# Kernel optimization log

Measured on AMD Instinct MI355X. Metric: run time of the kernel, lower is better.

The kernel has to match this reference:

```python
import jax, jax.numpy as jnp
import numpy as np

N = 50000
E = 400000
F_IN = 5
H = 8
C1, C2, C3 = 64, 32, 16
NEG_SLOPE = 0.2


def setup_inputs() -> dict:
    key = jax.random.key(0)
    ks = jax.random.split(key, 16)
    s = 0.1  # small init scale
    return {
        "x": jax.random.normal(ks[0], (N, F_IN), jnp.float32),
        "edge_index": jax.random.randint(ks[1], (2, E), 0, N, jnp.int64),
        "edge_weight": jax.random.uniform(ks[2], (E,), jnp.float32),
        "W1": jax.random.normal(ks[3], (F_IN, H * C1), jnp.float32) * s,
        "a_src1": jax.random.normal(ks[4], (H, C1), jnp.float32) * s,
        "a_dst1": jax.random.normal(ks[5], (H, C1), jnp.float32) * s,
        "b1": jnp.zeros((H * C1,), jnp.float32),
        "W2": jax.random.normal(ks[6], (H * C1, H * C2), jnp.float32) * s,
        "a_src2": jax.random.normal(ks[7], (H, C2), jnp.float32) * s,
        "a_dst2": jax.random.normal(ks[8], (H, C2), jnp.float32) * s,
        "b2": jnp.zeros((H * C2,), jnp.float32),
        "Wg": jax.random.normal(ks[9], (H * C2, C3), jnp.float32) * s,
        "bg": jnp.zeros((C3,), jnp.float32),
        "Wfc": jax.random.normal(ks[10], (C3, 1), jnp.float32) * s,
        "bfc": jnp.zeros((1,), jnp.float32),
    }


def _gat_layer(x, W, a_src, a_dst, b, src, dst, n, heads, ch):
    # PyG GATConv (concat=True), eval mode (dropout off), self-loops already in src/dst.
    h = (x @ W).reshape(n, heads, ch)                      # (N, H, C)
    e_s = jnp.sum(h * a_src, axis=-1)                      # (N, H)
    e_d = jnp.sum(h * a_dst, axis=-1)                      # (N, H)
    e = jax.nn.leaky_relu(e_s[src] + e_d[dst], NEG_SLOPE)  # (Etot, H)
    m = jax.ops.segment_max(e, dst, num_segments=n)
    m = jnp.where(jnp.isfinite(m), m, 0.0)                 # guard empty segments
    ex = jnp.exp(e - m[dst])
    den = jax.ops.segment_sum(ex, dst, num_segments=n)
    alpha = ex / (den[dst] + 1e-16)                        # softmax over in-edges
    out = jax.ops.segment_sum(h[src] * alpha[..., None], dst, num_segments=n)
    return out.reshape(n, heads * ch) + b


def _gcn_layer(x, W, b, src, dst, w_full, n):
    # PyG GCNConv with gcn_norm: D^{-1/2} A_hat D^{-1/2}, self-loop weight 1.
    deg = jax.ops.segment_sum(w_full, dst, num_segments=n)
    dinv = jnp.where(deg > 0, jax.lax.rsqrt(deg), 0.0)
    norm = dinv[src] * w_full * dinv[dst]                  # (Etot,)
    h = x @ W                                              # (N, C3)
    out = jax.ops.segment_sum(h[src] * norm[:, None], dst, num_segments=n)
    return out + b


def reference(x, edge_index, edge_weight, W1, a_src1, a_dst1, b1,
              W2, a_src2, a_dst2, b2, Wg, bg, Wfc, bfc):
    n = x.shape[0]
    loops = jnp.arange(n, dtype=edge_index.dtype)
    src = jnp.concatenate([edge_index[0], loops])
    dst = jnp.concatenate([edge_index[1], loops])
    w_full = jnp.concatenate([edge_weight, jnp.ones((n,), edge_weight.dtype)])

    h = _gat_layer(x, W1, a_src1, a_dst1, b1, src, dst, n, H, C1)
    h = jax.nn.elu(h)
    h = _gat_layer(h, W2, a_src2, a_dst2, b2, src, dst, n, H, C2)
    h = jax.nn.elu(h)
    h = _gcn_layer(h, Wg, bg, src, dst, w_full, n)
    h = jax.nn.elu(h)
    out = jax.nn.sigmoid(h @ Wfc + bfc)                    # (N, 1)
    return out
```

## Files before the change

### kernel.cpp

```cpp
#include <hip/hip_runtime.h>
#include <hip/hip_bf16.h>
#include <float.h>
#include <math.h>

#define N_NODES 50000
#define N_EDGES 400000
#define ETOT    (N_EDGES + N_NODES)
#define F_IN    5
#define HEADS   8
#define C1      64
#define C2      32
#define C3      16
#define HC1     (HEADS * C1)
#define HC2     (HEADS * C2)
#define NEG_SLOPE 0.2f
#define NCHUNK  ((N_NODES + 255) / 256)
#define NH8     (N_NODES * HEADS)
#define MPAD    (((N_NODES + 63) / 64) * 64)
#define GCOLS   (HC2 + 16)
#define PACKBLK ((GCOLS * HC1) / 256)
#define SCATBLK ((ETOT + 255) / 256)
#define ES1BLK  ((NH8 + 255) / 256)
#define DEGBLK  SCATBLK
#define XPBLK   ((N_NODES * 8 + 255) / 256)

typedef short bf16x8 __attribute__((ext_vector_type(8)));
typedef float f32x4  __attribute__((ext_vector_type(4)));
typedef unsigned short ushort_t;
typedef unsigned short ushort8_t __attribute__((ext_vector_type(8)));

__device__ __forceinline__ float eluf(float x) {
    return x > 0.f ? x : (expf(x) - 1.f);
}
__device__ __forceinline__ float bf2f(unsigned short u) {
    union { unsigned int i; float f; } v; v.i = ((unsigned int)u) << 16; return v.f;
}
__device__ __forceinline__ unsigned short f2bf(float f) {
    __hip_bfloat16 b = __float2bfloat16(f);
    return *(unsigned short*)&b;
}
__device__ __forceinline__ float softnum(float es, float ed) {
    float v = es + ed;
    v = v > 0.f ? v : NEG_SLOPE * v;
    return expf(v);
}

__global__ void k_deg(const int* __restrict__ ei, const float* __restrict__ ew,
                      int* degi, float* degf,
                      const float* __restrict__ x, float* __restrict__ xp8) {
    if (blockIdx.x < DEGBLK) {
        int i = blockIdx.x * blockDim.x + threadIdx.x;
        if (i >= ETOT) return;
        int d   = (i < N_EDGES) ? ei[N_EDGES + i] : (i - N_EDGES);
        float w = (i < N_EDGES) ? ew[i] : 1.f;
        atomicAdd(&degi[d], 1);
        atomicAdd(&degf[d], w);
    } else {
        int g = (blockIdx.x - DEGBLK) * 256 + threadIdx.x;
        if (g >= N_NODES * 8) return;
        int n = g >> 3, f = g & 7;
        xp8[g] = (f < F_IN) ? x[n * F_IN + f] : 0.f;
    }
}

__global__ void k_scan_a(const int* __restrict__ deg, int* __restrict__ part) {
    __shared__ int lds[256];
    int t = threadIdx.x;
    int i = blockIdx.x * 256 + t;
    lds[t] = (i < N_NODES) ? deg[i] : 0;
    __syncthreads();
    for (int off = 128; off >= 1; off >>= 1) {
        if (t < off) lds[t] += lds[t + off];
        __syncthreads();
    }
    if (t == 0) part[blockIdx.x] = lds[0];
}

__global__ void k_scan_b(int* part) {
    __shared__ int lds[256];
    int t = threadIdx.x;
    int v = (t < NCHUNK) ? part[t] : 0;
    lds[t] = v;
    __syncthreads();
    for (int off = 1; off < 256; off <<= 1) {
        int x = (t >= off) ? lds[t - off] : 0;
        __syncthreads();
        lds[t] += x;
        __syncthreads();
    }
    if (t < NCHUNK) part[t] = lds[t] - v;
}

__global__ void k_scan_c(const int* __restrict__ deg, const int* __restrict__ part,
                         int* __restrict__ offs,
                         const float* __restrict__ degf, float* __restrict__ dinv) {
    __shared__ int lds[256];
    int t = threadIdx.x;
    int i = blockIdx.x * 256 + t;
    int v = (i < N_NODES) ? deg[i] : 0;
    lds[t] = v;
    __syncthreads();
    for (int off = 1; off < 256; off <<= 1) {
        int x = (t >= off) ? lds[t - off] : 0;
        __syncthreads();
        lds[t] += x;
        __syncthreads();
    }
    int excl = part[blockIdx.x] + lds[t] - v;
    if (i < N_NODES) {
        offs[i] = excl;
        float dd = degf[i];
        dinv[i] = dd > 0.f ? rsqrtf(dd) : 0.f;
    }
    if (i == N_NODES - 1) offs[N_NODES] = excl + v;
}

__global__ void k_prep(const float* __restrict__ W2,
                       const float* __restrict__ a_src2, const float* __restrict__ a_dst2,
                       ushort_t* __restrict__ W2X,
                       const float* __restrict__ W1,
                       const float* __restrict__ a_src1, const float* __restrict__ a_dst1,
                       float* __restrict__ as1f, float* __restrict__ ad1f) {
    if (blockIdx.x < PACKBLK) {
        int idx = blockIdx.x * 256 + threadIdx.x;
        int c = idx >> 9;
        int k = idx & 511;
        float v;
        if (c < HC2) {
            v = W2[(size_t)k * HC2 + c];
        } else {
            int h = (c - HC2) & 7;
            const float* av = (c < HC2 + 8) ? a_src2 : a_dst2;
            v = 0.f;
#pragma unroll 8
            for (int j = 0; j < C2; j++)
                v += W2[(size_t)k * HC2 + h * C2 + j] * av[h * C2 + j];
        }
        W2X[idx] = f2bf(v);
    } else {
        int idx = threadIdx.x;
        if (idx >= HEADS * F_IN) return;
        int h = idx / F_IN, f = idx % F_IN;
        float s = 0.f, d = 0.f;
        for (int c = 0; c < C1; c++) {
            float w = W1[f * HC1 + h * C1 + c];
            s += w * a_src1[h * C1 + c];
            d += w * a_dst1[h * C1 + c];
        }
        as1f[idx] = s;
        ad1f[idx] = d;
    }
}

__global__ void k_scatter_es1(const int* __restrict__ ei, const int* __restrict__ offs,
                              int* cursor, int2* __restrict__ csr,
                              const float* __restrict__ ew, const float* __restrict__ dinv,
                              const float* __restrict__ x,
                              const float* __restrict__ as1f, const float* __restrict__ ad1f,
                              float* __restrict__ es, float* __restrict__ ed) {
    if (blockIdx.x < SCATBLK) {
        int i = blockIdx.x * 256 + threadIdx.x;
        if (i >= ETOT) return;
        int s, d;
        float w;
        if (i < N_EDGES) { s = ei[i]; d = ei[N_EDGES + i]; w = ew[i]; }
        else             { s = d = i - N_EDGES; w = 1.f; }
        float nrm = dinv[s] * w * dinv[d];
        int pos = offs[d] + atomicAdd(&cursor[d], 1);
        csr[pos] = make_int2(s, __float_as_int(nrm));
    } else {
        int g = (blockIdx.x - SCATBLK) * 256 + threadIdx.x;
        if (g >= NH8) return;
        int n = g >> 3, h = g & 7;
        float vs = 0.f, vd = 0.f;
#pragma unroll
        for (int f = 0; f < F_IN; f++) {
            float xv = x[n * F_IN + f];
            vs += xv * as1f[h * F_IN + f];
            vd += xv * ad1f[h * F_IN + f];
        }
        es[g] = vs;
        ed[g] = vd;
    }
}

__global__ void k_agg_x(const float* __restrict__ xp8,
                        const float* __restrict__ es1, const float* __restrict__ ed1,
                        const int* __restrict__ offs, const int2* __restrict__ csr,
                        float* __restrict__ aggx) {
    int g = blockIdx.x * blockDim.x + threadIdx.x;
    if (g >= NH8) return;
    int d = g >> 3, h = g & 7;
    float edv = ed1[g];
    int k0 = offs[d], k1 = offs[d + 1];
    float a0 = 0.f, a1 = 0.f, a2 = 0.f, a3 = 0.f, a4 = 0.f, exsum = 0.f;
    int k = k0;
    if (k + 1 < k1) {
        int2 c0 = csr[k], c1 = csr[k + 1];
        for (; k + 3 < k1; k += 2) {
            int2 n0 = csr[k + 2], n1 = csr[k + 3];
            float x0 = softnum(es1[c0.x * HEADS + h], edv);
            float x1 = softnum(es1[c1.x * HEADS + h], edv);
            float4 A0 = *(const float4*)(xp8 + (size_t)c0.x * 8);
            float  B0 = xp8[(size_t)c0.x * 8 + 4];
            float4 A1 = *(const float4*)(xp8 + (size_t)c1.x * 8);
            float  B1 = xp8[(size_t)c1.x * 8 + 4];
            a0 += x0 * A0.x + x1 * A1.x;
            a1 += x0 * A0.y + x1 * A1.y;
            a2 += x0 * A0.z + x1 * A1.z;
            a3 += x0 * A0.w + x1 * A1.w;
            a4 += x0 * B0   + x1 * B1;
            exsum += x0 + x1;
            c0 = n0; c1 = n1;
        }
        {
            float x0 = softnum(es1[c0.x * HEADS + h], edv);
            float x1 = softnum(es1[c1.x * HEADS + h], edv);
            float4 A0 = *(const float4*)(xp8 + (size_t)c0.x * 8);
            float  B0 = xp8[(size_t)c0.x * 8 + 4];
            float4 A1 = *(const float4*)(xp8 + (size_t)c1.x * 8);
            float  B1 = xp8[(size_t)c1.x * 8 + 4];
            a0 += x0 * A0.x + x1 * A1.x;
            a1 += x0 * A0.y + x1 * A1.y;
            a2 += x0 * A0.z + x1 * A1.z;
            a3 += x0 * A0.w + x1 * A1.w;
            a4 += x0 * B0   + x1 * B1;
            exsum += x0 + x1;
            k += 2;
        }
    }
    if (k < k1) {
        int2 c0 = csr[k];
        float x0 = softnum(es1[c0.x * HEADS + h], edv);
        float4 A0 = *(const float4*)(xp8 + (size_t)c0.x * 8);
        float  B0 = xp8[(size_t)c0.x * 8 + 4];
        a0 += x0 * A0.x;
        a1 += x0 * A0.y;
        a2 += x0 * A0.z;
        a3 += x0 * A0.w;
        a4 += x0 * B0;
        exsum += x0;
    }
    float inv = 1.f / (exsum + 1e-16f);
    aggx[0 * NH8 + g] = a0 * inv;
    aggx[1 * NH8 + g] = a1 * inv;
    aggx[2 * NH8 + g] = a2 * inv;
    aggx[3 * NH8 + g] = a3 * inv;
    aggx[4 * NH8 + g] = a4 * inv;
}

__global__ __launch_bounds__(256) void k_expand(const float* __restrict__ aggx,
                                                const float* __restrict__ W1,
                                                const float* __restrict__ b1,
                                                ushort_t* __restrict__ x2bf) {
    int wave = threadIdx.x >> 6;
    int j    = threadIdx.x & 63;
    int n    = blockIdx.x * 4 + wave;
    if (n >= N_NODES) return;
    int h = j >> 3;
    int g = n * HEADS + h;
    float av[F_IN];
#pragma unroll
    for (int f = 0; f < F_IN; f++) av[f] = aggx[f * NH8 + g];

    const float* w1p = W1 + j * 8;
    float4 s0 = *(const float4*)(b1 + j * 8);
    float4 s1 = *(const float4*)(b1 + j * 8 + 4);
#pragma unroll
    for (int f = 0; f < F_IN; f++) {
        float4 w0  = *(const float4*)(w1p + f * HC1);
        float4 w1v = *(const float4*)(w1p + f * HC1 + 4);
        s0.x += av[f] * w0.x;  s0.y += av[f] * w0.y;
        s0.z += av[f] * w0.z;  s0.w += av[f] * w0.w;
        s1.x += av[f] * w1v.x; s1.y += av[f] * w1v.y;
        s1.z += av[f] * w1v.z; s1.w += av[f] * w1v.w;
    }
    ushort8_t o;
    o[0] = f2bf(eluf(s0.x)); o[1] = f2bf(eluf(s0.y));
    o[2] = f2bf(eluf(s0.z)); o[3] = f2bf(eluf(s0.w));
    o[4] = f2bf(eluf(s1.x)); o[5] = f2bf(eluf(s1.y));
    o[6] = f2bf(eluf(s1.z)); o[7] = f2bf(eluf(s1.w));
    *(ushort8_t*)(x2bf + (size_t)n * HC1 + j * 8) = o;
}

__global__ __launch_bounds__(256, 3) void k_gemm_mfma(const short* __restrict__ A,
                                                      const short* __restrict__ W2X,
                                                      ushort_t* __restrict__ h2bf,
                                                      float* __restrict__ es2,
                                                      float* __restrict__ ed2) {
    __shared__ short Bs[GCOLS * 32];
    int t    = threadIdx.x;
    int wave = t >> 6;
    int lane = t & 63;
    int lo   = lane & 15;
    int quad = lane >> 4;
    int m0   = blockIdx.x * 64 + wave * 16;
    const short* ap = A + (size_t)(m0 + lo) * HC1 + quad * 8;

    f32x4 acc[17];
#pragma unroll
    for (int f = 0; f < 17; f++) acc[f] = (f32x4){0.f, 0.f, 0.f, 0.f};

    for (int idx = t; idx < GCOLS * 4; idx += 256) {
        int c = idx >> 2, q = idx & 3;
        int s = (q + c + (c >> 2)) & 3;
        *(bf16x8*)(Bs + c * 32 + s * 8) = *(const bf16x8*)(W2X + (size_t)c * HC1 + q * 8);
    }
    __syncthreads();

#pragma unroll 1
    for (int k0 = 0; k0 < HC1; k0 += 32) {
        int nk = k0 + 32;
        bf16x8 pre[5];
        if (nk < HC1) {
#pragma unroll
            for (int j = 0; j < 5; j++) {
                int idx = t + j * 256;
                if (idx < GCOLS * 4) {
                    int c = idx >> 2, q = idx & 3;
                    pre[j] = *(const bf16x8*)(W2X + (size_t)c * HC1 + nk + q * 8);
                }
            }
        }
        bf16x8 aF = *(const bf16x8*)(ap + k0);
#pragma unroll
        for (int f = 0; f < 17; f++) {
            int c = f * 16 + lo;
            int s = (quad + c + (c >> 2)) & 3;
            bf16x8 bF = *(const bf16x8*)(Bs + c * 32 + s * 8);
            acc[f] = __builtin_amdgcn_mfma_f32_16x16x32_bf16(aF, bF, acc[f], 0, 0, 0);
        }
        __syncthreads();
        if (nk < HC1) {
#pragma unroll
            for (int j = 0; j < 5; j++) {
                int idx = t + j * 256;
                if (idx < GCOLS * 4) {
                    int c = idx >> 2, q = idx & 3;
                    int s = (q + c + (c >> 2)) & 3;
                    *(bf16x8*)(Bs + c * 32 + s * 8) = pre[j];
                }
            }
            __syncthreads();
        }
    }

    int rowb = m0 + quad * 4;
#pragma unroll
    for (int f = 0; f < 16; f++) {
#pragma unroll
        for (int r = 0; r < 4; r++) {
            int row = rowb + r;
            if (row < N_NODES)
                h2bf[(size_t)row * HC2 + f * 16 + lo] = f2bf(acc[f][r]);
        }
    }
#pragma unroll
    for (int r = 0; r < 4; r++) {
        int row = rowb + r;
        if (row < N_NODES) {
            if (lo < 8) es2[row * HEADS + lo]       = acc[16][r];
            else        ed2[row * HEADS + (lo - 8)] = acc[16][r];
        }
    }
}

__global__ __launch_bounds__(256) void k_gat_agg2(const ushort_t* __restrict__ h2bf,
                                                  const float* __restrict__ es2,
                                                  const float* __restrict__ ed2,
                                                  const int* __restrict__ offs,
                                                  const int2* __restrict__ csr,
                                                  const float* __restrict__ b2,
                                                  ushort_t* __restrict__ x3bf) {
    int wave = threadIdx.x >> 6;
    int lane = threadIdx.x & 63;
    int d = blockIdx.x * 4 + wave;
    if (d >= N_NODES) return;
    int c4 = lane * 4;
    int h  = lane >> 3;
    float edv = ed2[d * HEADS + h];
    int k0 = offs[d], k1 = offs[d + 1];
    float acc0 = 0.f, acc1 = 0.f, acc2 = 0.f, acc3 = 0.f, exsum = 0.f;
    int k = k0;
    for (; k + 3 < k1; k += 4) {
        int2 e0 = csr[k], e1 = csr[k + 1], e2 = csr[k + 2], e3 = csr[k + 3];
        float r0 = es2[e0.x * HEADS + h];
        float r1 = es2[e1.x * HEADS + h];
        float r2 = es2[e2.x * HEADS + h];
        float r3 = es2[e3.x * HEADS + h];
        ushort4 v0 = *(const ushort4*)(h2bf + (size_t)e0.x * HC2 + c4);
        ushort4 v1 = *(const ushort4*)(h2bf + (size_t)e1.x * HC2 + c4);
        ushort4 v2 = *(const ushort4*)(h2bf + (size_t)e2.x * HC2 + c4);
        ushort4 v3 = *(const ushort4*)(h2bf + (size_t)e3.x * HC2 + c4);
        float x0 = softnum(r0, edv);
        float x1 = softnum(r1, edv);
        float x2 = softnum(r2, edv);
        float x3 = softnum(r3, edv);
        acc0 += x0 * bf2f(v0.x) + x1 * bf2f(v1.x) + x2 * bf2f(v2.x) + x3 * bf2f(v3.x);
        acc1 += x0 * bf2f(v0.y) + x1 * bf2f(v1.y) + x2 * bf2f(v2.y) + x3 * bf2f(v3.y);
        acc2 += x0 * bf2f(v0.z) + x1 * bf2f(v1.z) + x2 * bf2f(v2.z) + x3 * bf2f(v3.z);
        acc3 += x0 * bf2f(v0.w) + x1 * bf2f(v1.w) + x2 * bf2f(v2.w) + x3 * bf2f(v3.w);
        exsum += (x0 + x1) + (x2 + x3);
    }
    for (; k < k1; k++) {
        int2 e0 = csr[k];
        float x0 = softnum(es2[e0.x * HEADS + h], edv);
        ushort4 v0 = *(const ushort4*)(h2bf + (size_t)e0.x * HC2 + c4);
        acc0 += x0 * bf2f(v0.x);
        acc1 += x0 * bf2f(v0.y);
        acc2 += x0 * bf2f(v0.z);
        acc3 += x0 * bf2f(v0.w);
        exsum += x0;
    }
    float inv = 1.f / (exsum + 1e-16f);
    float4 bias = *(const float4*)(b2 + c4);
    ushort4 o;
    o.x = f2bf(eluf(acc0 * inv + bias.x));
    o.y = f2bf(eluf(acc1 * inv + bias.y));
    o.z = f2bf(eluf(acc2 * inv + bias.z));
    o.w = f2bf(eluf(acc3 * inv + bias.w));
    *(ushort4*)(x3bf + (size_t)d * HC2 + c4) = o;
}

__global__ __launch_bounds__(256) void k_hg(const ushort_t* __restrict__ x3bf,
                                            const float* __restrict__ Wg,
                                            float* __restrict__ hg) {
    __shared__ float xs[16 * 260];
    int n0 = blockIdx.x * 16;
    int t  = threadIdx.x;
    for (int q = t; q < 16 * HC2 / 4; q += 256) {
        int r  = q >> 6;
        int cc = (q & 63) * 4;
        int n  = n0 + r;
        ushort4 v = make_ushort4(0, 0, 0, 0);
        if (n < N_NODES) v = *(const ushort4*)(x3bf + (size_t)n * HC2 + cc);
        xs[r * 260 + cc + 0] = bf2f(v.x);
        xs[r * 260 + cc + 1] = bf2f(v.y);
        xs[r * 260 + cc + 2] = bf2f(v.z);
        xs[r * 260 + cc + 3] = bf2f(v.w);
    }
    __syncthreads();
    int r = t >> 4, c = t & 15;
    const float* xr = xs + r * 260;
    float acc = 0.f;
#pragma unroll 8
    for (int k = 0; k < HC2; k += 4) {
        float4 v = *(const float4*)(xr + k);
        acc += v.x * Wg[(k + 0) * C3 + c];
        acc += v.y * Wg[(k + 1) * C3 + c];
        acc += v.z * Wg[(k + 2) * C3 + c];
        acc += v.w * Wg[(k + 3) * C3 + c];
    }
    int n = n0 + r;
    if (n < N_NODES) hg[(size_t)n * C3 + c] = acc;
}

__global__ __launch_bounds__(256) void k_gcn_out(const float* __restrict__ hg,
                                                 const int* __restrict__ offs,
                                                 const int2* __restrict__ csr,
                                                 const float* __restrict__ bg,
                                                 const float* __restrict__ Wfc,
                                                 const float* __restrict__ bfc,
                                                 float* __restrict__ out) {
    int t = threadIdx.x;
    int r = t >> 4, c = t & 15;
    int d = blockIdx.x * 16 + r;
    float val = 0.f;
    if (d < N_NODES) {
        int k0 = offs[d], k1 = offs[d + 1];
        float acc = 0.f;
        int k = k0;
        if (k + 1 < k1) {
            int2 e0 = csr[k], e1 = csr[k + 1];
            for (; k + 3 < k1; k += 2) {
                int2 n0 = csr[k + 2], n1 = csr[k + 3];
                acc += hg[(size_t)e0.x * C3 + c] * __int_as_float(e0.y);
                acc += hg[(size_t)e1.x * C3 + c] * __int_as_float(e1.y);
                e0 = n0; e1 = n1;
            }
            acc += hg[(size_t)e0.x * C3 + c] * __int_as_float(e0.y);
            acc += hg[(size_t)e1.x * C3 + c] * __int_as_float(e1.y);
            k += 2;
        }
        if (k < k1) {
            int2 e0 = csr[k];
            acc += hg[(size_t)e0.x * C3 + c] * __int_as_float(e0.y);
        }
        val = eluf(acc + bg[c]);
    }
    float z = val * Wfc[c];
#pragma unroll
    for (int off = 8; off >= 1; off >>= 1) z += __shfl_xor(z, off, 16);
    if (c == 0 && d < N_NODES) out[d] = 1.f / (1.f + expf(-(z + bfc[0])));
}

extern "C" void kernel_launch(void* const* d_in, const int* in_sizes, int n_in,
                              void* d_out, int out_size, void* d_ws, size_t ws_size,
                              hipStream_t stream) {
    const float* x       = (const float*)d_in[0];
    const int*   ei      = (const int*)  d_in[1];
    const float* ew      = (const float*)d_in[2];
    const float* W1      = (const float*)d_in[3];
    const float* a_src1  = (const float*)d_in[4];
    const float* a_dst1  = (const float*)d_in[5];
    const float* b1      = (const float*)d_in[6];
    const float* W2      = (const float*)d_in[7];
    const float* a_src2  = (const float*)d_in[8];
    const float* a_dst2  = (const float*)d_in[9];
    const float* b2      = (const float*)d_in[10];
    const float* Wg      = (const float*)d_in[11];
    const float* bg      = (const float*)d_in[12];
    const float* Wfc     = (const float*)d_in[13];
    const float* bfc     = (const float*)d_in[14];
    float* out = (float*)d_out;

    char* w = (char*)d_ws;
    size_t off = 0;
    auto alloc = [&](size_t bytes) -> void* {
        void* p = w + off;
        off = (off + bytes + 255) & ~(size_t)255;
        return p;
    };
    ushort_t* x2bf = (ushort_t*)alloc((size_t)MPAD * HC1 * 2);
    ushort_t* W2X  = (ushort_t*)alloc((size_t)GCOLS * HC1 * 2);
    ushort_t* h2bf = (ushort_t*)alloc((size_t)N_NODES * HC2 * 2);
    ushort_t* x3bf = (ushort_t*)alloc((size_t)N_NODES * HC2 * 2);
    float* hg     = (float*)alloc((size_t)N_NODES * C3 * 4);
    float* aggx   = (float*)alloc((size_t)F_IN * NH8 * 4);
    float* es1    = (float*)alloc((size_t)NH8 * 4);
    float* ed1    = (float*)alloc((size_t)NH8 * 4);
    float* es2    = (float*)alloc((size_t)NH8 * 4);
    float* ed2    = (float*)alloc((size_t)NH8 * 4);
    float* as1f   = (float*)alloc((size_t)HEADS * F_IN * 4);
    float* ad1f   = (float*)alloc((size_t)HEADS * F_IN * 4);
    float* degf   = (float*)alloc((size_t)N_NODES * 4);
    int*   degi   = (int*)  alloc((size_t)N_NODES * 4);
    int*   cursor = (int*)  alloc((size_t)N_NODES * 4);
    char*  zero_end = w + off;
    int*   offs   = (int*)  alloc((size_t)(N_NODES + 1) * 4);
    int*   part   = (int*)  alloc(256 * 4);
    int2*  csr    = (int2*) alloc((size_t)ETOT * 8);
    float* dinv   = (float*)alloc((size_t)N_NODES * 4);
    float* xp8    = (float*)alloc((size_t)N_NODES * 8 * 4);

    const int T = 256;
    hipMemsetAsync(degf, 0, (size_t)(zero_end - (char*)degf), stream);
    k_deg<<<dim3(DEGBLK + XPBLK), dim3(T), 0, stream>>>(ei, ew, degi, degf, x, xp8);
    k_scan_a<<<dim3(NCHUNK), dim3(256), 0, stream>>>(degi, part);
    k_scan_b<<<dim3(1), dim3(256), 0, stream>>>(part);
    k_scan_c<<<dim3(NCHUNK), dim3(256), 0, stream>>>(degi, part, offs, degf, dinv);
    k_prep<<<dim3(PACKBLK + 1), dim3(256), 0, stream>>>(
        W2, a_src2, a_dst2, W2X, W1, a_src1, a_dst1, as1f, ad1f);
    k_scatter_es1<<<dim3(SCATBLK + ES1BLK), dim3(256), 0, stream>>>(
        ei, offs, cursor, csr, ew, dinv, x, as1f, ad1f, es1, ed1);

    k_agg_x<<<dim3((NH8 + T - 1) / T), dim3(T), 0, stream>>>(xp8, es1, ed1, offs, csr, aggx);
    k_expand<<<dim3((N_NODES + 3) / 4), dim3(256), 0, stream>>>(aggx, W1, b1, x2bf);

    k_gemm_mfma<<<dim3(MPAD / 64), dim3(256), 0, stream>>>(
        (const short*)x2bf, (const short*)W2X, h2bf, es2, ed2);
    k_gat_agg2<<<dim3((N_NODES + 3) / 4), dim3(256), 0, stream>>>(
        h2bf, es2, ed2, offs, csr, b2, x3bf);

    k_hg<<<dim3((N_NODES + 15) / 16), dim3(256), 0, stream>>>(x3bf, Wg, hg);
    k_gcn_out<<<dim3((N_NODES + 15) / 16), dim3(256), 0, stream>>>(
        hg, offs, csr, bg, Wfc, bfc, out);
}
```

Baseline: 310.1 us.

## Fuse setup kernels, merge layer-1 aggregation with expansion, shrink agg2 blocks

Merges the degree count, x padding, W2X packing and es1/ed1 projection into one init kernel, with the per-head attention vectors computed in shared memory per block. The layer-1 softmax aggregation and the expansion through W1 become one kernel, so the aggregated features pass through LDS instead of a global aggx buffer. This cuts two launches and a global round trip. The layer-2 aggregation kernel now runs 128-thread blocks of two nodes each, which may change occupancy and tail behaviour. Each es block recomputes the small attention projections, a small amount of redundant work.

```diff
diff --git a/kernel.cpp b/kernel.cpp
--- a/kernel.cpp
+++ b/kernel.cpp
@@ -21,8 +21,11 @@
 #define PACKBLK ((GCOLS * HC1) / 256)
 #define SCATBLK ((ETOT + 255) / 256)
 #define ES1BLK  ((NH8 + 255) / 256)
-#define DEGBLK  SCATBLK
 #define XPBLK   ((N_NODES * 8 + 255) / 256)
+#define INIT_DEG  SCATBLK
+#define INIT_XP   (INIT_DEG + XPBLK)
+#define INIT_W2X  (INIT_XP + PACKBLK)
+#define INIT_TOT  (INIT_W2X + ES1BLK)
 
 typedef short bf16x8 __attribute__((ext_vector_type(8)));
 typedef float f32x4  __attribute__((ext_vector_type(4)));
@@ -45,84 +48,32 @@
     return expf(v);
 }
 
-__global__ void k_deg(const int* __restrict__ ei, const float* __restrict__ ew,
-                      int* degi, float* degf,
-                      const float* __restrict__ x, float* __restrict__ xp8) {
-    if (blockIdx.x < DEGBLK) {
-        int i = blockIdx.x * blockDim.x + threadIdx.x;
+__global__ void k_init(const int* __restrict__ ei, const float* __restrict__ ew,
+                       int* degi, float* degf,
+                       const float* __restrict__ x, float* __restrict__ xp8,
+                       const float* __restrict__ W2,
+                       const float* __restrict__ a_src2, const float* __restrict__ a_dst2,
+                       ushort_t* __restrict__ W2X,
+                       const float* __restrict__ W1,
+                       const float* __restrict__ a_src1, const float* __restrict__ a_dst1,
+                       float* __restrict__ es, float* __restrict__ ed) {
+    __shared__ float asl[HEADS * F_IN], adl[HEADS * F_IN];
+    int b = blockIdx.x;
+    int t = threadIdx.x;
+    if (b < INIT_DEG) {
+        int i = b * 256 + t;
         if (i >= ETOT) return;
         int d   = (i < N_EDGES) ? ei[N_EDGES + i] : (i - N_EDGES);
         float w = (i < N_EDGES) ? ew[i] : 1.f;
         atomicAdd(&degi[d], 1);
         atomicAdd(&degf[d], w);
-    } else {
-        int g = (blockIdx.x - DEGBLK) * 256 + threadIdx.x;
+    } else if (b < INIT_XP) {
+        int g = (b - INIT_DEG) * 256 + t;
         if (g >= N_NODES * 8) return;
         int n = g >> 3, f = g & 7;
         xp8[g] = (f < F_IN) ? x[n * F_IN + f] : 0.f;
-    }
-}
-
-__global__ void k_scan_a(const int* __restrict__ deg, int* __restrict__ part) {
-    __shared__ int lds[256];
-    int t = threadIdx.x;
-    int i = blockIdx.x * 256 + t;
-    lds[t] = (i < N_NODES) ? deg[i] : 0;
-    __syncthreads();
-    for (int off = 128; off >= 1; off >>= 1) {
-        if (t < off) lds[t] += lds[t + off];
-        __syncthreads();
-    }
-    if (t == 0) part[blockIdx.x] = lds[0];
-}
-
-__global__ void k_scan_b(int* part) {
-    __shared__ int lds[256];
-    int t = threadIdx.x;
-    int v = (t < NCHUNK) ? part[t] : 0;
-    lds[t] = v;
-    __syncthreads();
-    for (int off = 1; off < 256; off <<= 1) {
-        int x = (t >= off) ? lds[t - off] : 0;
-        __syncthreads();
-        lds[t] += x;
-        __syncthreads();
-    }
-    if (t < NCHUNK) part[t] = lds[t] - v;
-}
-
-__global__ void k_scan_c(const int* __restrict__ deg, const int* __restrict__ part,
-                         int* __restrict__ offs,
-                         const float* __restrict__ degf, float* __restrict__ dinv) {
-    __shared__ int lds[256];
-    int t = threadIdx.x;
-    int i = blockIdx.x * 256 + t;
-    int v = (i < N_NODES) ? deg[i] : 0;
-    lds[t] = v;
-    __syncthreads();
-    for (int off = 1; off < 256; off <<= 1) {
-        int x = (t >= off) ? lds[t - off] : 0;
-        __syncthreads();
-        lds[t] += x;
-        __syncthreads();
-    }
-    int excl = part[blockIdx.x] + lds[t] - v;
-    if (i < N_NODES) {
-        offs[i] = excl;
-        float dd = degf[i];
-        dinv[i] = dd > 0.f ? rsqrtf(dd) : 0.f;
-    }
-    if (i == N_NODES - 1) offs[N_NODES] = excl + v;
-}
-
-__global__ void k_prep(const float* __restrict__ W2,
-                       const float* __restrict__ a_src2, const float* __restrict__ a_dst2,
-                       ushort_t* __restrict__ W2X,
-                       const float* __restrict__ W1,
-                       const float* __restrict__ a_src1, const float* __restrict__ a_dst1,
-                       float* __restrict__ as1f, float* __restrict__ ad1f) {
-    if (blockIdx.x < PACKBLK) {
-        int idx = blockIdx.x * 256 + threadIdx.x;
+    } else if (b < INIT_W2X) {
+        int idx = (b - INIT_XP) * 256 + t;
         int c = idx >> 9;
         int k = idx & 511;
         float v;
@@ -138,149 +89,203 @@
         }
         W2X[idx] = f2bf(v);
     } else {
-        int idx = threadIdx.x;
-        if (idx >= HEADS * F_IN) return;
-        int h = idx / F_IN, f = idx % F_IN;
-        float s = 0.f, d = 0.f;
-        for (int c = 0; c < C1; c++) {
-            float w = W1[f * HC1 + h * C1 + c];
-            s += w * a_src1[h * C1 + c];
-            d += w * a_dst1[h * C1 + c];
-        }
-        as1f[idx] = s;
-        ad1f[idx] = d;
-    }
-}
-
-__global__ void k_scatter_es1(const int* __restrict__ ei, const int* __restrict__ offs,
-                              int* cursor, int2* __restrict__ csr,
-                              const float* __restrict__ ew, const float* __restrict__ dinv,
-                              const float* __restrict__ x,
-                              const float* __restrict__ as1f, const float* __restrict__ ad1f,
-                              float* __restrict__ es, float* __restrict__ ed) {
-    if (blockIdx.x < SCATBLK) {
-        int i = blockIdx.x * 256 + threadIdx.x;
-        if (i >= ETOT) return;
-        int s, d;
-        float w;
-        if (i < N_EDGES) { s = ei[i]; d = ei[N_EDGES + i]; w = ew[i]; }
-        else             { s = d = i - N_EDGES; w = 1.f; }
-        float nrm = dinv[s] * w * dinv[d];
-        int pos = offs[d] + atomicAdd(&cursor[d], 1);
-        csr[pos] = make_int2(s, __float_as_int(nrm));
-    } else {
-        int g = (blockIdx.x - SCATBLK) * 256 + threadIdx.x;
-        if (g >= NH8) return;
-        int n = g >> 3, h = g & 7;
-        float vs = 0.f, vd = 0.f;
-#pragma unroll
-        for (int f = 0; f < F_IN; f++) {
-            float xv = x[n * F_IN + f];
-            vs += xv * as1f[h * F_IN + f];
-            vd += xv * ad1f[h * F_IN + f];
-        }
-        es[g] = vs;
-        ed[g] = vd;
-    }
-}
-
-__global__ void k_agg_x(const float* __restrict__ xp8,
-                        const float* __restrict__ es1, const float* __restrict__ ed1,
-                        const int* __restrict__ offs, const int2* __restrict__ csr,
-                        float* __restrict__ aggx) {
-    int g = blockIdx.x * blockDim.x + threadIdx.x;
-    if (g >= NH8) return;
-    int d = g >> 3, h = g & 7;
-    float edv = ed1[g];
-    int k0 = offs[d], k1 = offs[d + 1];
-    float a0 = 0.f, a1 = 0.f, a2 = 0.f, a3 = 0.f, a4 = 0.f, exsum = 0.f;
-    int k = k0;
-    if (k + 1 < k1) {
-        int2 c0 = csr[k], c1 = csr[k + 1];
-        for (; k + 3 < k1; k += 2) {
-            int2 n0 = csr[k + 2], n1 = csr[k + 3];
-            float x0 = softnum(es1[c0.x * HEADS + h], edv);
-            float x1 = softnum(es1[c1.x * HEADS + h], edv);
-            float4 A0 = *(const float4*)(xp8 + (size_t)c0.x * 8);
-            float  B0 = xp8[(size_t)c0.x * 8 + 4];
-            float4 A1 = *(const float4*)(xp8 + (size_t)c1.x * 8);
-            float  B1 = xp8[(size_t)c1.x * 8 + 4];
-            a0 += x0 * A0.x + x1 * A1.x;
-            a1 += x0 * A0.y + x1 * A1.y;
-            a2 += x0 * A0.z + x1 * A1.z;
-            a3 += x0 * A0.w + x1 * A1.w;
-            a4 += x0 * B0   + x1 * B1;
-            exsum += x0 + x1;
-            c0 = n0; c1 = n1;
-        }
-        {
-            float x0 = softnum(es1[c0.x * HEADS + h], edv);
-            float x1 = softnum(es1[c1.x * HEADS + h], edv);
-            float4 A0 = *(const float4*)(xp8 + (size_t)c0.x * 8);
-            float  B0 = xp8[(size_t)c0.x * 8 + 4];
-            float4 A1 = *(const float4*)(xp8 + (size_t)c1.x * 8);
-            float  B1 = xp8[(size_t)c1.x * 8 + 4];
-            a0 += x0 * A0.x + x1 * A1.x;
-            a1 += x0 * A0.y + x1 * A1.y;
-            a2 += x0 * A0.z + x1 * A1.z;
-            a3 += x0 * A0.w + x1 * A1.w;
-            a4 += x0 * B0   + x1 * B1;
-            exsum += x0 + x1;
-            k += 2;
-        }
-    }
-    if (k < k1) {
-        int2 c0 = csr[k];
-        float x0 = softnum(es1[c0.x * HEADS + h], edv);
-        float4 A0 = *(const float4*)(xp8 + (size_t)c0.x * 8);
-        float  B0 = xp8[(size_t)c0.x * 8 + 4];
-        a0 += x0 * A0.x;
-        a1 += x0 * A0.y;
-        a2 += x0 * A0.z;
-        a3 += x0 * A0.w;
-        a4 += x0 * B0;
-        exsum += x0;
-    }
-    float inv = 1.f / (exsum + 1e-16f);
-    aggx[0 * NH8 + g] = a0 * inv;
-    aggx[1 * NH8 + g] = a1 * inv;
-    aggx[2 * NH8 + g] = a2 * inv;
-    aggx[3 * NH8 + g] = a3 * inv;
-    aggx[4 * NH8 + g] = a4 * inv;
-}
-
-__global__ __launch_bounds__(256) void k_expand(const float* __restrict__ aggx,
+        if (t < HEADS * F_IN) {
+            int h = t / F_IN, f = t % F_IN;
+            float s = 0.f, dv = 0.f;
+            for (int c = 0; c < C1; c++) {
+                float wv = W1[f * HC1 + h * C1 + c];
+                s  += wv * a_src1[h * C1 + c];
+                dv += wv * a_dst1[h * C1 + c];
+            }
+            asl[t] = s;
+            adl[t] = dv;
+        }
+        __syncthreads();
+        int g = (b - INIT_W2X) * 256 + t;
+        if (g < NH8) {
+            int n = g >> 3, h = g & 7;
+            float vs = 0.f, vd = 0.f;
+#pragma unroll
+            for (int f = 0; f < F_IN; f++) {
+                float xv = x[n * F_IN + f];
+                vs += xv * asl[h * F_IN + f];
+                vd += xv * adl[h * F_IN + f];
+            }
+            es[g] = vs;
+            ed[g] = vd;
+        }
+    }
+}
+
+__global__ void k_scan_a(const int* __restrict__ deg, int* __restrict__ part) {
+    __shared__ int lds[256];
+    int t = threadIdx.x;
+    int i = blockIdx.x * 256 + t;
+    lds[t] = (i < N_NODES) ? deg[i] : 0;
+    __syncthreads();
+    for (int off = 128; off >= 1; off >>= 1) {
+        if (t < off) lds[t] += lds[t + off];
+        __syncthreads();
+    }
+    if (t == 0) part[blockIdx.x] = lds[0];
+}
+
+__global__ void k_scan_b(int* part) {
+    __shared__ int lds[256];
+    int t = threadIdx.x;
+    int v = (t < NCHUNK) ? part[t] : 0;
+    lds[t] = v;
+    __syncthreads();
+    for (int off = 1; off < 256; off <<= 1) {
+        int x = (t >= off) ? lds[t - off] : 0;
+        __syncthreads();
+        lds[t] += x;
+        __syncthreads();
+    }
+    if (t < NCHUNK) part[t] = lds[t] - v;
+}
+
+__global__ void k_scan_c(const int* __restrict__ deg, const int* __restrict__ part,
+                         int* __restrict__ offs,
+                         const float* __restrict__ degf, float* __restrict__ dinv) {
+    __shared__ int lds[256];
+    int t = threadIdx.x;
+    int i = blockIdx.x * 256 + t;
+    int v = (i < N_NODES) ? deg[i] : 0;
+    lds[t] = v;
+    __syncthreads();
+    for (int off = 1; off < 256; off <<= 1) {
+        int x = (t >= off) ? lds[t - off] : 0;
+        __syncthreads();
+        lds[t] += x;
+        __syncthreads();
+    }
+    int excl = part[blockIdx.x] + lds[t] - v;
+    if (i < N_NODES) {
+        offs[i] = excl;
+        float dd = degf[i];
+        dinv[i] = dd > 0.f ? rsqrtf(dd) : 0.f;
+    }
+    if (i == N_NODES - 1) offs[N_NODES] = excl + v;
+}
+
+__global__ void k_scatter(const int* __restrict__ ei, const int* __restrict__ offs,
+                          int* cursor, int2* __restrict__ csr,
+                          const float* __restrict__ ew, const float* __restrict__ dinv) {
+    int i = blockIdx.x * 256 + threadIdx.x;
+    if (i >= ETOT) return;
+    int s, d;
+    float w;
+    if (i < N_EDGES) { s = ei[i]; d = ei[N_EDGES + i]; w = ew[i]; }
+    else             { s = d = i - N_EDGES; w = 1.f; }
+    float nrm = dinv[s] * w * dinv[d];
+    int pos = offs[d] + atomicAdd(&cursor[d], 1);
+    csr[pos] = make_int2(s, __float_as_int(nrm));
+}
+
+__global__ __launch_bounds__(256) void k_aggexp(const float* __restrict__ xp8,
+                                                const float* __restrict__ es1,
+                                                const float* __restrict__ ed1,
+                                                const int* __restrict__ offs,
+                                                const int2* __restrict__ csr,
                                                 const float* __restrict__ W1,
                                                 const float* __restrict__ b1,
                                                 ushort_t* __restrict__ x2bf) {
-    int wave = threadIdx.x >> 6;
-    int j    = threadIdx.x & 63;
-    int n    = blockIdx.x * 4 + wave;
-    if (n >= N_NODES) return;
+    __shared__ float ax[256 * F_IN];
+    int t = threadIdx.x;
+    int g = blockIdx.x * 256 + t;
+    if (g < NH8) {
+        int d = g >> 3, h = g & 7;
+        float edv = ed1[g];
+        int k0 = offs[d], k1 = offs[d + 1];
+        float a0 = 0.f, a1 = 0.f, a2 = 0.f, a3 = 0.f, a4 = 0.f, exsum = 0.f;
+        int k = k0;
+        if (k + 1 < k1) {
+            int2 c0 = csr[k], c1 = csr[k + 1];
+            for (; k + 3 < k1; k += 2) {
+                int2 n0 = csr[k + 2], n1 = csr[k + 3];
+                float x0 = softnum(es1[c0.x * HEADS + h], edv);
+                float x1 = softnum(es1[c1.x * HEADS + h], edv);
+                float4 A0 = *(const float4*)(xp8 + (size_t)c0.x * 8);
+                float  B0 = xp8[(size_t)c0.x * 8 + 4];
+                float4 A1 = *(const float4*)(xp8 + (size_t)c1.x * 8);
+                float  B1 = xp8[(size_t)c1.x * 8 + 4];
+                a0 += x0 * A0.x + x1 * A1.x;
+                a1 += x0 * A0.y + x1 * A1.y;
+                a2 += x0 * A0.z + x1 * A1.z;
+                a3 += x0 * A0.w + x1 * A1.w;
+                a4 += x0 * B0   + x1 * B1;
+                exsum += x0 + x1;
+                c0 = n0; c1 = n1;
+            }
+            {
+                float x0 = softnum(es1[c0.x * HEADS + h], edv);
+                float x1 = softnum(es1[c1.x * HEADS + h], edv);
+                float4 A0 = *(const float4*)(xp8 + (size_t)c0.x * 8);
+                float  B0 = xp8[(size_t)c0.x * 8 + 4];
+                float4 A1 = *(const float4*)(xp8 + (size_t)c1.x * 8);
+                float  B1 = xp8[(size_t)c1.x * 8 + 4];
+                a0 += x0 * A0.x + x1 * A1.x;
+                a1 += x0 * A0.y + x1 * A1.y;
+                a2 += x0 * A0.z + x1 * A1.z;
+                a3 += x0 * A0.w + x1 * A1.w;
+                a4 += x0 * B0   + x1 * B1;
+                exsum += x0 + x1;
+                k += 2;
+            }
+        }
+        if (k < k1) {
+            int2 c0 = csr[k];
+            float x0 = softnum(es1[c0.x * HEADS + h], edv);
+            float4 A0 = *(const float4*)(xp8 + (size_t)c0.x * 8);
+            float  B0 = xp8[(size_t)c0.x * 8 + 4];
+            a0 += x0 * A0.x;
+            a1 += x0 * A0.y;
+            a2 += x0 * A0.z;
+            a3 += x0 * A0.w;
+            a4 += x0 * B0;
+            exsum += x0;
+        }
+        float inv = 1.f / (exsum + 1e-16f);
+        float* ap = ax + t * F_IN;
+        ap[0] = a0 * inv;
+        ap[1] = a1 * inv;
+        ap[2] = a2 * inv;
+        ap[3] = a3 * inv;
+        ap[4] = a4 * inv;
+    }
+    __syncthreads();
+    int wave = t >> 6, j = t & 63;
+    int n0 = blockIdx.x * 32;
     int h = j >> 3;
-    int g = n * HEADS + h;
-    float av[F_IN];
-#pragma unroll
-    for (int f = 0; f < F_IN; f++) av[f] = aggx[f * NH8 + g];
-
     const float* w1p = W1 + j * 8;
-    float4 s0 = *(const float4*)(b1 + j * 8);
-    float4 s1 = *(const float4*)(b1 + j * 8 + 4);
-#pragma unroll
-    for (int f = 0; f < F_IN; f++) {
-        float4 w0  = *(const float4*)(w1p + f * HC1);
-        float4 w1v = *(const float4*)(w1p + f * HC1 + 4);
-        s0.x += av[f] * w0.x;  s0.y += av[f] * w0.y;
-        s0.z += av[f] * w0.z;  s0.w += av[f] * w0.w;
-        s1.x += av[f] * w1v.x; s1.y += av[f] * w1v.y;
-        s1.z += av[f] * w1v.z; s1.w += av[f] * w1v.w;
-    }
-    ushort8_t o;
-    o[0] = f2bf(eluf(s0.x)); o[1] = f2bf(eluf(s0.y));
-    o[2] = f2bf(eluf(s0.z)); o[3] = f2bf(eluf(s0.w));
-    o[4] = f2bf(eluf(s1.x)); o[5] = f2bf(eluf(s1.y));
-    o[6] = f2bf(eluf(s1.z)); o[7] = f2bf(eluf(s1.w));
-    *(ushort8_t*)(x2bf + (size_t)n * HC1 + j * 8) = o;
+#pragma unroll 1
+    for (int it = 0; it < 8; ++it) {
+        int nl = wave * 8 + it;
+        int n = n0 + nl;
+        if (n >= N_NODES) break;
+        const float* ap = ax + (nl * 8 + h) * F_IN;
+        float av[F_IN];
+#pragma unroll
+        for (int f = 0; f < F_IN; f++) av[f] = ap[f];
+        float4 s0 = *(const float4*)(b1 + j * 8);
+        float4 s1 = *(const float4*)(b1 + j * 8 + 4);
+#pragma unroll
+        for (int f = 0; f < F_IN; f++) {
+            float4 w0  = *(const float4*)(w1p + f * HC1);
+            float4 w1v = *(const float4*)(w1p + f * HC1 + 4);
+            s0.x += av[f] * w0.x;  s0.y += av[f] * w0.y;
+            s0.z += av[f] * w0.z;  s0.w += av[f] * w0.w;
+            s1.x += av[f] * w1v.x; s1.y += av[f] * w1v.y;
+            s1.z += av[f] * w1v.z; s1.w += av[f] * w1v.w;
+        }
+        ushort8_t o;
+        o[0] = f2bf(eluf(s0.x)); o[1] = f2bf(eluf(s0.y));
+        o[2] = f2bf(eluf(s0.z)); o[3] = f2bf(eluf(s0.w));
+        o[4] = f2bf(eluf(s1.x)); o[5] = f2bf(eluf(s1.y));
+        o[6] = f2bf(eluf(s1.z)); o[7] = f2bf(eluf(s1.w));
+        *(ushort8_t*)(x2bf + (size_t)n * HC1 + j * 8) = o;
+    }
 }
 
 __global__ __launch_bounds__(256, 3) void k_gemm_mfma(const short* __restrict__ A,
@@ -365,7 +370,7 @@
     }
 }
 
-__global__ __launch_bounds__(256) void k_gat_agg2(const ushort_t* __restrict__ h2bf,
+__global__ __launch_bounds__(128) void k_gat_agg2(const ushort_t* __restrict__ h2bf,
                                                   const float* __restrict__ es2,
                                                   const float* __restrict__ ed2,
                                                   const int* __restrict__ offs,
@@ -374,7 +379,7 @@
                                                   ushort_t* __restrict__ x3bf) {
     int wave = threadIdx.x >> 6;
     int lane = threadIdx.x & 63;
-    int d = blockIdx.x * 4 + wave;
+    int d = blockIdx.x * 2 + wave;
     if (d >= N_NODES) return;
     int c4 = lane * 4;
     int h  = lane >> 3;
@@ -526,13 +531,10 @@
     ushort_t* h2bf = (ushort_t*)alloc((size_t)N_NODES * HC2 * 2);
     ushort_t* x3bf = (ushort_t*)alloc((size_t)N_NODES * HC2 * 2);
     float* hg     = (float*)alloc((size_t)N_NODES * C3 * 4);
-    float* aggx   = (float*)alloc((size_t)F_IN * NH8 * 4);
     float* es1    = (float*)alloc((size_t)NH8 * 4);
     float* ed1    = (float*)alloc((size_t)NH8 * 4);
     float* es2    = (float*)alloc((size_t)NH8 * 4);
     float* ed2    = (float*)alloc((size_t)NH8 * 4);
-    float* as1f   = (float*)alloc((size_t)HEADS * F_IN * 4);
-    float* ad1f   = (float*)alloc((size_t)HEADS * F_IN * 4);
     float* degf   = (float*)alloc((size_t)N_NODES * 4);
     int*   degi   = (int*)  alloc((size_t)N_NODES * 4);
     int*   cursor = (int*)  alloc((size_t)N_NODES * 4);
@@ -543,23 +545,21 @@
     float* dinv   = (float*)alloc((size_t)N_NODES * 4);
     float* xp8    = (float*)alloc((size_t)N_NODES * 8 * 4);
 
-    const int T = 256;
     hipMemsetAsync(degf, 0, (size_t)(zero_end - (char*)degf), stream);
-    k_deg<<<dim3(DEGBLK + XPBLK), dim3(T), 0, stream>>>(ei, ew, degi, degf, x, xp8);
+    k_init<<<dim3(INIT_TOT), dim3(256), 0, stream>>>(
+        ei, ew, degi, degf, x, xp8, W2, a_src2, a_dst2, W2X,
+        W1, a_src1, a_dst1, es1, ed1);
     k_scan_a<<<dim3(NCHUNK), dim3(256), 0, stream>>>(degi, part);
     k_scan_b<<<dim3(1), dim3(256), 0, stream>>>(part);
     k_scan_c<<<dim3(NCHUNK), dim3(256), 0, stream>>>(degi, part, offs, degf, dinv);
-    k_prep<<<dim3(PACKBLK + 1), dim3(256), 0, stream>>>(
-        W2, a_src2, a_dst2, W2X, W1, a_src1, a_dst1, as1f, ad1f);
-    k_scatter_es1<<<dim3(SCATBLK + ES1BLK), dim3(256), 0, stream>>>(
-        ei, offs, cursor, csr, ew, dinv, x, as1f, ad1f, es1, ed1);
-
-    k_agg_x<<<dim3((NH8 + T - 1) / T), dim3(T), 0, stream>>>(xp8, es1, ed1, offs, csr, aggx);
-    k_expand<<<dim3((N_NODES + 3) / 4), dim3(256), 0, stream>>>(aggx, W1, b1, x2bf);
+    k_scatter<<<dim3(SCATBLK), dim3(256), 0, stream>>>(ei, offs, cursor, csr, ew, dinv);
+
+    k_aggexp<<<dim3(ES1BLK), dim3(256), 0, stream>>>(
+        xp8, es1, ed1, offs, csr, W1, b1, x2bf);
 
     k_gemm_mfma<<<dim3(MPAD / 64), dim3(256), 0, stream>>>(
         (const short*)x2bf, (const short*)W2X, h2bf, es2, ed2);
-    k_gat_agg2<<<dim3((N_NODES + 3) / 4), dim3(256), 0, stream>>>(
+    k_gat_agg2<<<dim3((N_NODES + 1) / 2), dim3(128), 0, stream>>>(
         h2bf, es2, ed2, offs, csr, b2, x3bf);
 
     k_hg<<<dim3((N_NODES + 15) / 16), dim3(256), 0, stream>>>(x3bf, Wg, hg);
```

New measurement: 310.4 us. Within noise of the previous version (+0.1%).
